# Optimization experiments

Measured on AMD Instinct MI355X. Metric: run time of the kernel, lower is better.

## Reference

```python
import jax, jax.numpy as jnp
import numpy as np
from functools import partial

VOCAB = 1000
HID = 512
EPS = 1e-3  # Keras BatchNorm default epsilon


def _conv1d(x, w, stride):
    # x: [B,T,C_in], w: [K,C_in,C_out]
    return jax.lax.conv_general_dilated(x, w, window_strides=(stride,), padding='SAME',
                                        dimension_numbers=('NWC', 'WIO', 'NWC'))


def setup_inputs() -> dict:
    key = jax.random.key(0)
    ks = jax.random.split(key, 8)
    s = lambda *sh: 1.0 / np.sqrt(sh[-2] if len(sh) > 1 else sh[-1])
    return {
        'x': jax.random.normal(ks[0], (32, 1600, 80), jnp.float32),
        'y_true': jax.random.randint(ks[1], (32, 201), 0, VOCAB),
        'bn_gamma': jnp.ones((80,), jnp.float32),
        'bn_beta': jnp.zeros((80,), jnp.float32),
        'conv0_w': jax.random.normal(ks[2], (5, 80, 512), jnp.float32) * 0.05,
        'conv0_b': jnp.zeros((512,), jnp.float32),
        'tcr_w': jax.random.normal(ks[3], (4, 5, 512, 512), jnp.float32) * 0.02,
        'tcr_b': jnp.zeros((4, 512), jnp.float32),
        'gru_kernel': jax.random.normal(ks[4], (VOCAB, 3 * HID), jnp.float32) * 0.03,
        'gru_rec_kernel': jax.random.normal(ks[5], (HID, 3 * HID), jnp.float32) * 0.04,
        'gru_bias': jnp.zeros((2, 3 * HID), jnp.float32),
        'fc_w': jax.random.normal(ks[6], (2 * HID, VOCAB), jnp.float32) * 0.03,
        'fc_b': jnp.zeros((VOCAB,), jnp.float32),
    }


def reference(x, y_true, bn_gamma, bn_beta, conv0_w, conv0_b, tcr_w, tcr_b,
              gru_kernel, gru_rec_kernel, gru_bias, fc_w, fc_b):
    # ---- Encoder ----
    # BatchNorm (training mode: batch statistics over batch & time)
    mean = jnp.mean(x, axis=(0, 1))
    var = jnp.var(x, axis=(0, 1))
    h = (x - mean) * jax.lax.rsqrt(var + EPS) * bn_gamma + bn_beta
    # strided Conv1D + relu -> [B, T=800, 512]
    h = jax.nn.relu(_conv1d(h, conv0_w, 2) + conv0_b)
    # Temporal conv residual blocks: out = relu(conv(x)) + x
    for i in range(tcr_w.shape[0]):
        h = jax.nn.relu(_conv1d(h, tcr_w[i], 1) + tcr_b[i]) + h
    enc = h  # [B, T, D]
    B = enc.shape[0]

    # ---- Decoder (teacher forcing, training branch) ----
    y_oh = jax.nn.one_hot(y_true, VOCAB, dtype=jnp.float32)  # [B, U+1, V]
    inputs = jnp.transpose(y_oh[:, :-1, :], (1, 0, 2))       # [U, B, V]
    bi, br = gru_bias[0], gru_bias[1]

    def step(hstate, y_u):
        # Keras GRUCell (reset_after=True)
        mx = y_u @ gru_kernel + bi
        mh = hstate @ gru_rec_kernel + br
        xz, xr, xh = jnp.split(mx, 3, axis=-1)
        hz, hr, hh = jnp.split(mh, 3, axis=-1)
        z = jax.nn.sigmoid(xz + hz)
        r = jax.nn.sigmoid(xr + hr)
        cand = jnp.tanh(xh + r * hh)
        h_new = z * hstate + (1.0 - z) * cand
        # Dot-product attention over encoder states
        scores = jnp.einsum('bd,btd->bt', h_new, enc)
        alpha = jax.nn.softmax(scores, axis=-1)
        ctx = jnp.einsum('bt,btd->bd', alpha, enc)
        # output projection with softmax activation
        y_pred = jax.nn.softmax(jnp.concatenate([h_new, ctx], axis=1) @ fc_w + fc_b, axis=-1)
        return h_new, y_pred

    h0 = jnp.zeros((B, HID), jnp.float32)
    _, outs = jax.lax.scan(step, h0, inputs)  # [U, B, V]
    return jnp.transpose(outs, (1, 0, 2))     # [B, U, V]
```

## Files before the change

kernel.cpp:

```cpp
#include <hip/hip_runtime.h>
#include <cstdint>

typedef _Float16 f16;
typedef __attribute__((ext_vector_type(2))) _Float16 f16x2;
typedef __attribute__((ext_vector_type(8))) _Float16 f16x8;
typedef __attribute__((ext_vector_type(4))) float f32x4;
typedef __attribute__((ext_vector_type(2))) float f32x2;
typedef __attribute__((ext_vector_type(8))) unsigned short us8;
typedef __attribute__((ext_vector_type(4))) int i32x4;

#define NB   32
#define TIN  1600
#define CIN  80
#define TOUT 800
#define DH   512
#define NV   1000
#define NU   200
#define TXP  1604
#define THP  804
#define EPSB 1e-3f
#define EWG  248

__device__ __forceinline__ void st_sys_f16(f16* p, float v)
{
    f16 h = (f16)v;
    short s; __builtin_memcpy(&s, &h, 2);
    int si = (int)s;
    asm volatile("global_store_short %0, %1, off sc0 sc1"
                 :: "v"(p), "v"(si) : "memory");
}
__device__ __forceinline__ void st_sys_i32(int* p, int v)
{
    asm volatile("global_store_dword %0, %1, off sc0 sc1"
                 :: "v"(p), "v"(v) : "memory");
}

__device__ __forceinline__ void poll8(const int* fl, int target)
{
    i32x4 a, b;
    while (true) {
        asm volatile("global_load_dwordx4 %0, %2, off sc1\n\t"
                     "global_load_dwordx4 %1, %3, off sc1\n\t"
                     "s_waitcnt vmcnt(0)"
                     : "=&v"(a), "=&v"(b)
                     : "v"(fl), "v"(fl + 4)
                     : "memory");
        if (a.x == target && a.y == target && a.z == target && a.w == target &&
            b.x == target && b.y == target && b.z == target && b.w == target) break;
        __builtin_amdgcn_s_sleep(1);
    }
}

__device__ __forceinline__ float fast_tanh(float x)
{
    return 1.f - 2.f / (__expf(2.f * x) + 1.f);
}

__global__ void init_zero(float* gsum, float* gsumsq,
                          int* flags, int* lcnt, f16* xpad, f16* hbufA, f16* hbufB)
{
    int tid = blockIdx.x * 256 + threadIdx.x;
    int stride = gridDim.x * 256;
    if (blockIdx.x == 0) {
        if (threadIdx.x < 80) { gsum[threadIdx.x] = 0.f; gsumsq[threadIdx.x] = 0.f; }
        if (threadIdx.x >= 128 && threadIdx.x < 136) lcnt[threadIdx.x - 128] = 0;
    }
    for (int i = tid; i < NU * 8; i += stride) flags[i] = 0;
    for (int i = tid; i < NB * 4 * CIN; i += stride) {
        int b = i / (4 * CIN), rr = (i / CIN) % 4, c = i % CIN;
        int row = (rr == 0) ? 0 : (1600 + rr);
        xpad[((long)b * TXP + row) * CIN + c] = (f16)0.f;
    }
    for (int i = tid; i < 2 * NB * 4 * DH; i += stride) {
        int q = i; int buf = q / (NB * 4 * DH); q %= NB * 4 * DH;
        int b = q / (4 * DH); int rr = (q / DH) % 4; int dd = q % DH;
        int row = (rr < 2) ? rr : (800 + rr);
        f16* hb = buf ? hbufB : hbufA;
        hb[((long)b * THP + row) * DH + dd] = (f16)0.f;
    }
}

__global__ void transpose_f32_f16(const float* __restrict__ in, int R, int C,
                                  f16* __restrict__ out, int outRows, int outCols)
{
    __shared__ float t[32][33];
    int c0 = blockIdx.x * 32, r0 = blockIdx.y * 32;
    int x = threadIdx.x & 31, y = threadIdx.x >> 5;
    for (int i = y; i < 32; i += 8) {
        int r = r0 + i, c = c0 + x;
        t[i][x] = (r < R && c < C) ? in[(long)r * C + c] : 0.0f;
    }
    __syncthreads();
    for (int i = y; i < 32; i += 8) {
        int orow = c0 + i, ocol = r0 + x;
        if (orow < outRows && ocol < outCols)
            out[(long)orow * outCols + ocol] = (f16)t[x][i];
    }
}

__global__ void bn_stats(const float* __restrict__ x, float* gsum, float* gsumsq)
{
    __shared__ float ls[240], ls2[240];
    const float* base = x + (long)blockIdx.x * 200 * CIN;
    int tid = threadIdx.x;
    if (tid < 240) {
        int c = tid % 80, rg = tid / 80;
        float s = 0.f, s2 = 0.f;
        for (int r = rg; r < 200; r += 3) {
            float v = base[r * CIN + c];
            s += v; s2 += v * v;
        }
        ls[tid] = s; ls2[tid] = s2;
    }
    __syncthreads();
    if (tid < 80) {
        atomicAdd(&gsum[tid],   ls[tid] + ls[tid + 80] + ls[tid + 160]);
        atomicAdd(&gsumsq[tid], ls2[tid] + ls2[tid + 80] + ls2[tid + 160]);
    }
}

__global__ void bn_apply(const float* __restrict__ x, const float* __restrict__ gsum,
                         const float* __restrict__ gsumsq, const float* __restrict__ gamma,
                         const float* __restrict__ beta, f16* __restrict__ xpad)
{
    long idx = (long)blockIdx.x * 256 + threadIdx.x;
    if (idx >= (long)NB * TIN * CIN) return;
    int c = (int)(idx % CIN);
    long bt = idx / CIN;
    int t = (int)(bt % TIN); int b = (int)(bt / TIN);
    float mean = gsum[c] * (1.f / 51200.f);
    float var  = gsumsq[c] * (1.f / 51200.f) - mean * mean;
    float sc = gamma[c] * rsqrtf(var + EPSB);
    float sh = beta[c] - mean * sc;
    xpad[((long)b * TXP + t + 1) * CIN + c] = (f16)(x[idx] * sc + sh);
}

template<int MODE>
__launch_bounds__(256)
__global__ void gemm16(const f16* __restrict__ Ab, long strideA, long slabA,
                       const f16* __restrict__ Bb, long strideB, long slabB,
                       int M, int N, int Kchunks,
                       const float* __restrict__ bias,
                       float* __restrict__ outF)
{
    __shared__ f16 As[64][72];
    __shared__ f16 Bs[128][72];
    const int b = blockIdx.z;
    const f16* Abase = Ab + (long)b * slabA;
    const f16* Bbase = Bb + (long)b * slabB;
    const int m0 = blockIdx.x * 64, n0 = blockIdx.y * 128;
    const int tid = threadIdx.x;
    const int lane = tid & 63, wv = tid >> 6;
    const int lm = lane & 15, lk = lane >> 4;

    f32x4 vzero = {0.f, 0.f, 0.f, 0.f};
    f32x4 acc[4][2];
#pragma unroll
    for (int i = 0; i < 4; i++) { acc[i][0] = vzero; acc[i][1] = vzero; }

    const int srow = tid >> 3, scol = (tid & 7) * 8;

    for (int kc = 0; kc < Kchunks; kc++) {
        int kb = kc * 64;
#pragma unroll
        for (int p = 0; p < 2; p++) {
            int r = srow + p * 32;
            int m = m0 + r; if (m > M - 1) m = M - 1;
            *(us8*)&As[r][scol] = *(const us8*)(Abase + (long)m * strideA + kb + scol);
        }
#pragma unroll
        for (int p = 0; p < 4; p++) {
            int r = srow + p * 32;
            int n = n0 + r; if (n > N - 1) n = N - 1;
            *(us8*)&Bs[r][scol] = *(const us8*)(Bbase + (long)n * strideB + kb + scol);
        }
        __syncthreads();
#pragma unroll
        for (int ks = 0; ks < 2; ks++) {
            f16x8 af[4], bf[2];
#pragma unroll
            for (int mt = 0; mt < 4; mt++)
                af[mt] = *(const f16x8*)&As[mt * 16 + lm][ks * 32 + lk * 8];
#pragma unroll
            for (int nt = 0; nt < 2; nt++)
                bf[nt] = *(const f16x8*)&Bs[wv * 32 + nt * 16 + lm][ks * 32 + lk * 8];
#pragma unroll
            for (int mt = 0; mt < 4; mt++)
#pragma unroll
                for (int nt = 0; nt < 2; nt++)
                    acc[mt][nt] = __builtin_amdgcn_mfma_f32_16x16x32_f16(af[mt], bf[nt], acc[mt][nt], 0, 0, 0);
        }
        __syncthreads();
    }
#pragma unroll
    for (int mt = 0; mt < 4; mt++) {
#pragma unroll
        for (int nt = 0; nt < 2; nt++) {
            int n = n0 + wv * 32 + nt * 16 + lm;
#pragma unroll
            for (int reg = 0; reg < 4; reg++) {
                int m = m0 + mt * 16 + lk * 4 + reg;
                if (m >= M || n >= N) continue;
                float v = acc[mt][nt][reg];
                if (MODE == 2) {
                    outF[((long)b * NU + m) * 800 + n] = v;
                } else {
                    v += bias[n];
                    int u = m >> 5, bb = m & 31;
                    outF[((long)bb * NU + u) * 1000 + n] = v;
                }
            }
        }
    }
}

__device__ void enc_layer(int eb, int tid,
                          const f16* __restrict__ Ab, long strideA, long slabA,
                          const f16* __restrict__ Bb, long strideB,
                          int Kchunks, const float* __restrict__ bias,
                          const f16* __restrict__ resid, f16* __restrict__ outH,
                          long slabRO, f16 As[][72], f16 Bs[][72])
{
    const int lane = tid & 63, wv = tid >> 6;
    const int lm = lane & 15, lk = lane >> 4;
    const int srow = tid >> 3, scol = (tid & 7) * 8;
    f32x4 vzero = {0.f, 0.f, 0.f, 0.f};

    for (int t = eb; t < 1664; t += EWG) {
        int b = t / 52, rem = t - b * 52;
        int m0 = (rem >> 2) * 64, n0 = (rem & 3) * 128;
        const f16* Abase = Ab + (long)b * slabA;

        f32x4 acc[4][2];
#pragma unroll
        for (int i = 0; i < 4; i++) { acc[i][0] = vzero; acc[i][1] = vzero; }

        for (int kc = 0; kc < Kchunks; kc++) {
            int kb = kc * 64;
#pragma unroll
            for (int p = 0; p < 2; p++) {
                int r = srow + p * 32;
                int m = m0 + r; if (m > 799) m = 799;
                *(us8*)&As[r][scol] = *(const us8*)(Abase + (long)m * strideA + kb + scol);
            }
#pragma unroll
            for (int p = 0; p < 4; p++) {
                int r = srow + p * 32;
                *(us8*)&Bs[r][scol] = *(const us8*)(Bb + (long)(n0 + r) * strideB + kb + scol);
            }
            __syncthreads();
#pragma unroll
            for (int ks = 0; ks < 2; ks++) {
                f16x8 af[4], bf[2];
#pragma unroll
                for (int mt = 0; mt < 4; mt++)
                    af[mt] = *(const f16x8*)&As[mt * 16 + lm][ks * 32 + lk * 8];
#pragma unroll
                for (int nt = 0; nt < 2; nt++)
                    bf[nt] = *(const f16x8*)&Bs[wv * 32 + nt * 16 + lm][ks * 32 + lk * 8];
#pragma unroll
                for (int mt = 0; mt < 4; mt++)
#pragma unroll
                    for (int nt = 0; nt < 2; nt++)
                        acc[mt][nt] = __builtin_amdgcn_mfma_f32_16x16x32_f16(af[mt], bf[nt], acc[mt][nt], 0, 0, 0);
            }
            __syncthreads();
        }
#pragma unroll
        for (int mt = 0; mt < 4; mt++) {
#pragma unroll
            for (int nt = 0; nt < 2; nt++) {
                int n = n0 + wv * 32 + nt * 16 + lm;
#pragma unroll
                for (int reg = 0; reg < 4; reg++) {
                    int m = m0 + mt * 16 + lk * 4 + reg;
                    if (m >= 800) continue;
                    float v = acc[mt][nt][reg] + bias[n];
                    v = v > 0.f ? v : 0.f;
                    if (resid) v += (float)resid[(long)b * slabRO + (long)(2 + m) * DH + n];
                    outH[(long)b * slabRO + (long)(2 + m) * DH + n] = (f16)v;
                }
            }
        }
    }
}

__launch_bounds__(256, 1)
__global__ void enc_gru(const f16* __restrict__ wrecT, const float* __restrict__ gk,
                        const float* __restrict__ gbias, const int* __restrict__ ytrue,
                        f16* __restrict__ Hc, int* __restrict__ flags,
                        const f16* __restrict__ xpad, const f16* __restrict__ w0T,
                        const float* __restrict__ b0, const f16* __restrict__ tcrT,
                        const float* __restrict__ tcrb,
                        f16* __restrict__ hbufA, f16* __restrict__ hbufB,
                        int* __restrict__ lcnt)
{
    const int tid = threadIdx.x;

    if (blockIdx.x < 8) {
        __shared__ int yl[NU * 32];
        const int lane = tid & 63, wv = tid >> 6;
        const int gw = (int)blockIdx.x * 4 + wv;
        const int lm = lane & 15, lk = lane >> 4;
        const int j = gw * 16 + lm;

        for (int i = tid; i < NU * 32; i += 256) {
            int b = i / NU, u = i - b * NU;
            yl[u * 32 + b] = ytrue[b * 201 + u];
        }

        f16x8 wf[3][16];
#pragma unroll
        for (int g = 0; g < 3; g++)
#pragma unroll
            for (int ks = 0; ks < 16; ks++)
                wf[g][ks] = *(const f16x8*)&wrecT[(long)(g * 512 + j) * 512 + ks * 32 + lk * 8];

        const float biz = gbias[j],        bir = gbias[512 + j],        bic = gbias[1024 + j];
        const float brz = gbias[1536 + j], brr = gbias[1536 + 512 + j], brc = gbias[1536 + 1024 + j];
        f32x4 vzero = {0.f, 0.f, 0.f, 0.f};

        __syncthreads();

        float hold[8];
        float nxz[8], nxr[8], nxh[8], mxz[8], mxr[8], mxh[8];
#pragma unroll
        for (int s = 0; s < 8; s++) {
            hold[s] = 0.f;
            int b = ((s >> 2) << 4) + lk * 4 + (s & 3);
            const float* gkr = gk + (long)yl[b] * 1536;
            nxz[s] = gkr[j]; nxr[s] = gkr[512 + j]; nxh[s] = gkr[1024 + j];
        }

        for (int u = 0; u < NU; u++) {
            int up = (u < NU - 1) ? u + 1 : u;
#pragma unroll
            for (int s = 0; s < 8; s++) {
                int b = ((s >> 2) << 4) + lk * 4 + (s & 3);
                const float* gkr = gk + (long)yl[up * 32 + b] * 1536;
                mxz[s] = gkr[j]; mxr[s] = gkr[512 + j]; mxh[s] = gkr[1024 + j];
            }

            f32x4 acc[3][2];
#pragma unroll
            for (int g = 0; g < 3; g++) { acc[g][0] = vzero; acc[g][1] = vzero; }

            if (u > 0) {
                poll8(flags + (u - 1) * 8, u);
                const f16* hrow = Hc + (long)(u - 1) * 32 * 1024 + lk * 8;
#pragma unroll
                for (int ks = 0; ks < 16; ks++) {
                    f16x8 a0 = *(const f16x8*)(hrow + (long)lm * 1024 + ks * 32);
                    f16x8 a1 = *(const f16x8*)(hrow + (long)(16 + lm) * 1024 + ks * 32);
#pragma unroll
                    for (int g = 0; g < 3; g++) {
                        acc[g][0] = __builtin_amdgcn_mfma_f32_16x16x32_f16(a0, wf[g][ks], acc[g][0], 0, 0, 0);
                        acc[g][1] = __builtin_amdgcn_mfma_f32_16x16x32_f16(a1, wf[g][ks], acc[g][1], 0, 0, 0);
                    }
                }
            }

#pragma unroll
            for (int mt = 0; mt < 2; mt++) {
#pragma unroll
                for (int reg = 0; reg < 4; reg++) {
                    int s = mt * 4 + reg;
                    int b = mt * 16 + lk * 4 + reg;
                    float hz = acc[0][mt][reg] + brz;
                    float hr = acc[1][mt][reg] + brr;
                    float hh = acc[2][mt][reg] + brc;
                    float z = 1.f / (1.f + __expf(-(nxz[s] + biz + hz)));
                    float r = 1.f / (1.f + __expf(-(nxr[s] + bir + hr)));
                    float cd = fast_tanh(nxh[s] + bic + r * hh);
                    float hnew = z * hold[s] + (1.f - z) * cd;
                    hold[s] = hnew;
                    st_sys_f16(&Hc[((long)u * 32 + b) * 1024 + j], hnew);
                }
            }
#pragma unroll
            for (int s = 0; s < 8; s++) { nxz[s] = mxz[s]; nxr[s] = mxr[s]; nxh[s] = mxh[s]; }

            if (u < NU - 1) {
                asm volatile("s_waitcnt vmcnt(0)" ::: "memory");
                __syncthreads();
                if (tid == 0) st_sys_i32(&flags[u * 8 + (int)blockIdx.x], u + 1);
            }
        }
        asm volatile("s_waitcnt vmcnt(0)" ::: "memory");
        return;
    }

    __shared__ f16 As[64][72];
    __shared__ f16 Bs[128][72];
    const int eb = (int)blockIdx.x - 8;

    enc_layer(eb, tid, xpad, 160, (long)TXP * CIN, w0T, 448, 7, b0,
              nullptr, hbufA, (long)THP * DH, As, Bs);

    const f16* tin = hbufA; f16* tout = hbufB;
    for (int L = 0; L < 4; L++) {
        __syncthreads();
        if (tid == 0) {
            __hip_atomic_fetch_add(&lcnt[L], 1, __ATOMIC_RELEASE, __HIP_MEMORY_SCOPE_AGENT);
            while (__hip_atomic_load(&lcnt[L], __ATOMIC_RELAXED, __HIP_MEMORY_SCOPE_AGENT) < EWG)
                __builtin_amdgcn_s_sleep(8);
            (void)__hip_atomic_load(&lcnt[L], __ATOMIC_ACQUIRE, __HIP_MEMORY_SCOPE_AGENT);
        }
        __syncthreads();

        enc_layer(eb, tid, tin, 512, (long)THP * DH, tcrT + (size_t)L * 512 * 2560, 2560,
                  40, tcrb + L * 512, tin, tout, (long)THP * DH, As, Bs);
        const f16* t2 = tout; tout = (f16*)tin; tin = t2;
    }
}

__global__ void row_softmax(float* __restrict__ base, int len)
{
    float* s = base + (long)blockIdx.x * len;
    int tid = threadIdx.x;
    float v[4]; float mx = -1e30f;
#pragma unroll
    for (int i = 0; i < 4; i++) {
        int idx = tid + i * 256;
        v[i] = (idx < len) ? s[idx] : -1e30f;
        mx = fmaxf(mx, v[i]);
    }
#pragma unroll
    for (int off = 32; off; off >>= 1) mx = fmaxf(mx, __shfl_xor(mx, off));
    __shared__ float red[4], red2[4];
    if ((tid & 63) == 0) red[tid >> 6] = mx;
    __syncthreads();
    mx = fmaxf(fmaxf(red[0], red[1]), fmaxf(red[2], red[3]));
    float sum = 0.f;
#pragma unroll
    for (int i = 0; i < 4; i++) { v[i] = __expf(v[i] - mx); sum += v[i]; }
#pragma unroll
    for (int off = 32; off; off >>= 1) sum += __shfl_xor(sum, off);
    if ((tid & 63) == 0) red2[tid >> 6] = sum;
    __syncthreads();
    sum = red2[0] + red2[1] + red2[2] + red2[3];
    float inv = 1.f / sum;
#pragma unroll
    for (int i = 0; i < 4; i++) {
        int idx = tid + i * 256;
        if (idx < len) s[idx] = v[i] * inv;
    }
}

__global__ void ctx_kernel(const float* __restrict__ alpha, const f16* __restrict__ enc,
                           f16* __restrict__ Hc)
{
    __shared__ float al[800][18];
    int b = blockIdx.x, ut = blockIdx.y;
    int u0 = ut * 16;
    int tid = threadIdx.x;
    for (int ul = 0; ul < 16; ul++) {
        int u = u0 + ul;
        if (u < NU) {
            const float* arow = alpha + ((long)b * NU + u) * 800;
            for (int t = tid; t < 800; t += 256) al[t][ul] = arow[t];
        } else {
            for (int t = tid; t < 800; t += 256) al[t][ul] = 0.f;
        }
    }
    __syncthreads();
    int d0 = tid * 2;
    float a0[16], a1[16];
#pragma unroll
    for (int i = 0; i < 16; i++) { a0[i] = 0.f; a1[i] = 0.f; }
    const f16* encb = enc + ((long)b * THP + 2) * DH + d0;
    for (int t = 0; t < 800; t++) {
        f16x2 e = *(const f16x2*)&encb[(long)t * DH];
        float f0 = (float)e.x, f1 = (float)e.y;
#pragma unroll
        for (int g = 0; g < 8; g++) {
            f32x2 ap = *(const f32x2*)&al[t][2 * g];
            a0[2 * g]     += ap.x * f0; a0[2 * g + 1] += ap.y * f0;
            a1[2 * g]     += ap.x * f1; a1[2 * g + 1] += ap.y * f1;
        }
    }
#pragma unroll
    for (int ul = 0; ul < 16; ul++) {
        int u = u0 + ul;
        if (u < NU) {
            Hc[((long)u * 32 + b) * 1024 + 512 + d0]     = (f16)a0[ul];
            Hc[((long)u * 32 + b) * 1024 + 512 + d0 + 1] = (f16)a1[ul];
        }
    }
}

extern "C" void kernel_launch(void* const* d_in, const int* in_sizes, int n_in,
                              void* d_out, int out_size, void* d_ws, size_t ws_size,
                              hipStream_t stream)
{
    const float* x     = (const float*)d_in[0];
    const int*   ytrue = (const int*)d_in[1];
    const float* gamma = (const float*)d_in[2];
    const float* beta  = (const float*)d_in[3];
    const float* w0    = (const float*)d_in[4];
    const float* b0    = (const float*)d_in[5];
    const float* tcrw  = (const float*)d_in[6];
    const float* tcrb  = (const float*)d_in[7];
    const float* gk    = (const float*)d_in[8];
    const float* grk   = (const float*)d_in[9];
    const float* gbias = (const float*)d_in[10];
    const float* fcw   = (const float*)d_in[11];
    const float* fcb   = (const float*)d_in[12];
    float* out = (float*)d_out;
    (void)in_sizes; (void)n_in; (void)out_size; (void)ws_size;

    char* ws = (char*)d_ws;
    size_t o = 0;
    auto alloc = [&](size_t bytes) { size_t r = o; o += (bytes + 255) & ~(size_t)255; return r; };
    f16*   xpad   = (f16*)(ws + alloc((size_t)NB * TXP * CIN * 2));
    f16*   hbufA  = (f16*)(ws + alloc((size_t)NB * THP * DH * 2));
    f16*   hbufB  = (f16*)(ws + alloc((size_t)NB * THP * DH * 2));
    f16*   Hc     = (f16*)(ws + alloc((size_t)NU * NB * 1024 * 2));
    float* scores = (float*)(ws + alloc((size_t)NB * NU * 800 * 4));
    f16*   w0T    = (f16*)(ws + alloc((size_t)512 * 448 * 2));
    f16*   tcrT   = (f16*)(ws + alloc((size_t)4 * 512 * 2560 * 2));
    f16*   wrecT  = (f16*)(ws + alloc((size_t)1536 * 512 * 2));
    f16*   fcT    = (f16*)(ws + alloc((size_t)1024 * 1024 * 2));
    float* gsum   = (float*)(ws + alloc(80 * 4));
    float* gsumsq = (float*)(ws + alloc(80 * 4));
    int*   flags  = (int*)(ws + alloc(NU * 8 * 4));
    int*   lcnt   = (int*)(ws + alloc(64));

    init_zero<<<64, 256, 0, stream>>>(gsum, gsumsq, flags, lcnt, xpad, hbufA, hbufB);
    transpose_f32_f16<<<dim3(16, 14), 256, 0, stream>>>(w0, 400, 512, w0T, 512, 448);
    for (int i = 0; i < 4; i++)
        transpose_f32_f16<<<dim3(16, 80), 256, 0, stream>>>(tcrw + (size_t)i * 2560 * 512, 2560, 512,
                                                            tcrT + (size_t)i * 512 * 2560, 512, 2560);
    transpose_f32_f16<<<dim3(48, 16), 256, 0, stream>>>(grk, 512, 1536, wrecT, 1536, 512);
    transpose_f32_f16<<<dim3(32, 32), 256, 0, stream>>>(fcw, 1024, 1000, fcT, 1024, 1024);

    bn_stats<<<256, 256, 0, stream>>>(x, gsum, gsumsq);
    bn_apply<<<16000, 256, 0, stream>>>(x, gsum, gsumsq, gamma, beta, xpad);

    enc_gru<<<8 + EWG, 256, 0, stream>>>(wrecT, gk, gbias, ytrue, Hc, flags,
                                         xpad, w0T, b0, tcrT, tcrb, hbufA, hbufB, lcnt);
    const f16* enc = hbufA;

    gemm16<2><<<dim3(4, 7, 32), 256, 0, stream>>>(Hc, 32 * 1024, 1024, enc + 2 * DH, 512, (long)THP * DH,
        200, 800, 8, nullptr, scores);
    row_softmax<<<6400, 256, 0, stream>>>(scores, 800);
    ctx_kernel<<<dim3(32, 13), 256, 0, stream>>>(scores, enc, Hc);

    gemm16<3><<<dim3(100, 8, 1), 256, 0, stream>>>(Hc, 1024, 0, fcT, 1024, 0,
        6400, 1000, 16, fcb, out);
    row_softmax<<<6400, 256, 0, stream>>>(out, 1000);
}
```

Before: 1.860 ms.

## Replace GRU flag barriers with NaN-sentinel polling on hidden-state data

The per-step flag handshake between the 8 GRU blocks is removed. Hc is pre-filled with f16 NaN sentinels, and consumers poll the hidden-state rows directly until no NaN remains, then feed those loaded values straight into the MFMAs. This drops the __syncthreads, the waitcnt and the flag store on every step, and merges the wait with the data load. The risk is reading torn or partially visible data. It relies on per-element store visibility and on the GRU never producing a NaN itself, and init must now write the whole Hc buffer.

Measured after the change: 1.673 ms. 10.1% less time.

```diff
diff --git a/kernel.cpp b/kernel.cpp
--- a/kernel.cpp
+++ b/kernel.cpp
@@ -29,24 +29,43 @@
     asm volatile("global_store_short %0, %1, off sc0 sc1"
                  :: "v"(p), "v"(si) : "memory");
 }
-__device__ __forceinline__ void st_sys_i32(int* p, int v)
-{
-    asm volatile("global_store_dword %0, %1, off sc0 sc1"
-                 :: "v"(p), "v"(v) : "memory");
-}
-
-__device__ __forceinline__ void poll8(const int* fl, int target)
-{
-    i32x4 a, b;
+
+__device__ __forceinline__ void poll_h16(const f16* base, f16x8 v[16])
+{
     while (true) {
-        asm volatile("global_load_dwordx4 %0, %2, off sc1\n\t"
-                     "global_load_dwordx4 %1, %3, off sc1\n\t"
-                     "s_waitcnt vmcnt(0)"
-                     : "=&v"(a), "=&v"(b)
-                     : "v"(fl), "v"(fl + 4)
-                     : "memory");
-        if (a.x == target && a.y == target && a.z == target && a.w == target &&
-            b.x == target && b.y == target && b.z == target && b.w == target) break;
+        asm volatile(
+            "global_load_dwordx4 %0, %16, off sc1\n\t"
+            "global_load_dwordx4 %1, %16, off offset:64 sc1\n\t"
+            "global_load_dwordx4 %2, %16, off offset:128 sc1\n\t"
+            "global_load_dwordx4 %3, %16, off offset:192 sc1\n\t"
+            "global_load_dwordx4 %4, %16, off offset:256 sc1\n\t"
+            "global_load_dwordx4 %5, %16, off offset:320 sc1\n\t"
+            "global_load_dwordx4 %6, %16, off offset:384 sc1\n\t"
+            "global_load_dwordx4 %7, %16, off offset:448 sc1\n\t"
+            "global_load_dwordx4 %8, %16, off offset:512 sc1\n\t"
+            "global_load_dwordx4 %9, %16, off offset:576 sc1\n\t"
+            "global_load_dwordx4 %10, %16, off offset:640 sc1\n\t"
+            "global_load_dwordx4 %11, %16, off offset:704 sc1\n\t"
+            "global_load_dwordx4 %12, %16, off offset:768 sc1\n\t"
+            "global_load_dwordx4 %13, %16, off offset:832 sc1\n\t"
+            "global_load_dwordx4 %14, %16, off offset:896 sc1\n\t"
+            "global_load_dwordx4 %15, %16, off offset:960 sc1\n\t"
+            "s_waitcnt vmcnt(0)"
+            : "=&v"(v[0]), "=&v"(v[1]), "=&v"(v[2]), "=&v"(v[3]),
+              "=&v"(v[4]), "=&v"(v[5]), "=&v"(v[6]), "=&v"(v[7]),
+              "=&v"(v[8]), "=&v"(v[9]), "=&v"(v[10]), "=&v"(v[11]),
+              "=&v"(v[12]), "=&v"(v[13]), "=&v"(v[14]), "=&v"(v[15])
+            : "v"(base)
+            : "memory");
+        f16x8 s0 = v[0] + v[1],   s1 = v[2] + v[3];
+        f16x8 s2 = v[4] + v[5],   s3 = v[6] + v[7];
+        f16x8 s4 = v[8] + v[9],   s5 = v[10] + v[11];
+        f16x8 s6 = v[12] + v[13], s7 = v[14] + v[15];
+        s0 += s1; s2 += s3; s4 += s5; s6 += s7;
+        s0 += s2; s4 += s6; s0 += s4;
+        float r = (float)s0[0] + (float)s0[1] + (float)s0[2] + (float)s0[3]
+                + (float)s0[4] + (float)s0[5] + (float)s0[6] + (float)s0[7];
+        if (!__any(r != r)) return;
         __builtin_amdgcn_s_sleep(1);
     }
 }
@@ -57,7 +76,8 @@
 }
 
 __global__ void init_zero(float* gsum, float* gsumsq,
-                          int* flags, int* lcnt, f16* xpad, f16* hbufA, f16* hbufB)
+                          int* lcnt, f16* xpad, f16* hbufA, f16* hbufB,
+                          f16* Hc)
 {
     int tid = blockIdx.x * 256 + threadIdx.x;
     int stride = gridDim.x * 256;
@@ -65,7 +85,6 @@
         if (threadIdx.x < 80) { gsum[threadIdx.x] = 0.f; gsumsq[threadIdx.x] = 0.f; }
         if (threadIdx.x >= 128 && threadIdx.x < 136) lcnt[threadIdx.x - 128] = 0;
     }
-    for (int i = tid; i < NU * 8; i += stride) flags[i] = 0;
     for (int i = tid; i < NB * 4 * CIN; i += stride) {
         int b = i / (4 * CIN), rr = (i / CIN) % 4, c = i % CIN;
         int row = (rr == 0) ? 0 : (1600 + rr);
@@ -78,6 +97,11 @@
         f16* hb = buf ? hbufB : hbufA;
         hb[((long)b * THP + row) * DH + dd] = (f16)0.f;
     }
+    us8 sent;
+#pragma unroll
+    for (int e = 0; e < 8; e++) sent[e] = 0x7FFFu;
+    for (int i = tid; i < 6400 * 64; i += stride)
+        *(us8*)&Hc[(long)(i >> 6) * 1024 + (i & 63) * 8] = sent;
 }
 
 __global__ void transpose_f32_f16(const float* __restrict__ in, int R, int C,
@@ -288,7 +312,7 @@
 __launch_bounds__(256, 1)
 __global__ void enc_gru(const f16* __restrict__ wrecT, const float* __restrict__ gk,
                         const float* __restrict__ gbias, const int* __restrict__ ytrue,
-                        f16* __restrict__ Hc, int* __restrict__ flags,
+                        f16* __restrict__ Hc,
                         const f16* __restrict__ xpad, const f16* __restrict__ w0T,
                         const float* __restrict__ b0, const f16* __restrict__ tcrT,
                         const float* __restrict__ tcrb,
@@ -313,8 +337,10 @@
 #pragma unroll
         for (int g = 0; g < 3; g++)
 #pragma unroll
-            for (int ks = 0; ks < 16; ks++)
+            for (int ks = 0; ks < 16; ks++) {
                 wf[g][ks] = *(const f16x8*)&wrecT[(long)(g * 512 + j) * 512 + ks * 32 + lk * 8];
+                asm volatile("" : "+v"(wf[g][ks]));
+            }
 
         const float biz = gbias[j],        bir = gbias[512 + j],        bic = gbias[1024 + j];
         const float brz = gbias[1536 + j], brr = gbias[1536 + 512 + j], brc = gbias[1536 + 1024 + j];
@@ -346,17 +372,24 @@
             for (int g = 0; g < 3; g++) { acc[g][0] = vzero; acc[g][1] = vzero; }
 
             if (u > 0) {
-                poll8(flags + (u - 1) * 8, u);
-                const f16* hrow = Hc + (long)(u - 1) * 32 * 1024 + lk * 8;
-#pragma unroll
-                for (int ks = 0; ks < 16; ks++) {
-                    f16x8 a0 = *(const f16x8*)(hrow + (long)lm * 1024 + ks * 32);
-                    f16x8 a1 = *(const f16x8*)(hrow + (long)(16 + lm) * 1024 + ks * 32);
-#pragma unroll
-                    for (int g = 0; g < 3; g++) {
-                        acc[g][0] = __builtin_amdgcn_mfma_f32_16x16x32_f16(a0, wf[g][ks], acc[g][0], 0, 0, 0);
-                        acc[g][1] = __builtin_amdgcn_mfma_f32_16x16x32_f16(a1, wf[g][ks], acc[g][1], 0, 0, 0);
-                    }
+                const f16* baseA = Hc + ((long)(u - 1) * 32 + lm) * 1024 + lk * 8;
+                {
+                    f16x8 va[16];
+                    poll_h16(baseA, va);
+#pragma unroll
+                    for (int ks = 0; ks < 16; ks++)
+#pragma unroll
+                        for (int g = 0; g < 3; g++)
+                            acc[g][0] = __builtin_amdgcn_mfma_f32_16x16x32_f16(va[ks], wf[g][ks], acc[g][0], 0, 0, 0);
+                }
+                {
+                    f16x8 vb[16];
+                    poll_h16(baseA + 16 * 1024, vb);
+#pragma unroll
+                    for (int ks = 0; ks < 16; ks++)
+#pragma unroll
+                        for (int g = 0; g < 3; g++)
+                            acc[g][1] = __builtin_amdgcn_mfma_f32_16x16x32_f16(vb[ks], wf[g][ks], acc[g][1], 0, 0, 0);
                 }
             }
 
@@ -379,12 +412,6 @@
             }
 #pragma unroll
             for (int s = 0; s < 8; s++) { nxz[s] = mxz[s]; nxr[s] = mxr[s]; nxh[s] = mxh[s]; }
-
-            if (u < NU - 1) {
-                asm volatile("s_waitcnt vmcnt(0)" ::: "memory");
-                __syncthreads();
-                if (tid == 0) st_sys_i32(&flags[u * 8 + (int)blockIdx.x], u + 1);
-            }
         }
         asm volatile("s_waitcnt vmcnt(0)" ::: "memory");
         return;
@@ -523,10 +550,9 @@
     f16*   fcT    = (f16*)(ws + alloc((size_t)1024 * 1024 * 2));
     float* gsum   = (float*)(ws + alloc(80 * 4));
     float* gsumsq = (float*)(ws + alloc(80 * 4));
-    int*   flags  = (int*)(ws + alloc(NU * 8 * 4));
     int*   lcnt   = (int*)(ws + alloc(64));
 
-    init_zero<<<64, 256, 0, stream>>>(gsum, gsumsq, flags, lcnt, xpad, hbufA, hbufB);
+    init_zero<<<64, 256, 0, stream>>>(gsum, gsumsq, lcnt, xpad, hbufA, hbufB, Hc);
     transpose_f32_f16<<<dim3(16, 14), 256, 0, stream>>>(w0, 400, 512, w0T, 512, 448);
     for (int i = 0; i < 4; i++)
         transpose_f32_f16<<<dim3(16, 80), 256, 0, stream>>>(tcrw + (size_t)i * 2560 * 512, 2560, 512,
@@ -537,7 +563,7 @@
     bn_stats<<<256, 256, 0, stream>>>(x, gsum, gsumsq);
     bn_apply<<<16000, 256, 0, stream>>>(x, gsum, gsumsq, gamma, beta, xpad);
 
-    enc_gru<<<8 + EWG, 256, 0, stream>>>(wrecT, gk, gbias, ytrue, Hc, flags,
+    enc_gru<<<8 + EWG, 256, 0, stream>>>(wrecT, gk, gbias, ytrue, Hc,
                                          xpad, w0T, b0, tcrT, tcrb, hbufA, hbufB, lcnt);
     const f16* enc = hbufA;
 
```
